# Kernel optimization log

Hardware: AMD Instinct MI355X
Metric: run time of the kernel (lower is better)

## Reference

```python
import jax, jax.numpy as jnp
import numpy as np

EPS = 1e-5  # torch nn.LayerNorm default

def layer_norm(x, g, b):
    mu = jnp.mean(x, axis=-1, keepdims=True)
    var = jnp.mean((x - mu) ** 2, axis=-1, keepdims=True)  # biased, as torch
    return (x - mu) * jax.lax.rsqrt(var + EPS) * g + b

def quantum_circuit(v):
    # RX(v_w) per wire -> <Z_w> = cos(v_w); RZ(params) is diagonal phase (no effect
    # on Z probabilities); CNOT chain makes bit w = XOR of bits 0..w, hence
    # <Z_w> = prod_{k<=w} cos(v_k). Exact closed form of the PennyLane circuit.
    return jnp.cumprod(jnp.cos(v), axis=-1)

def setup_inputs() -> dict:
    key = jax.random.key(0)
    ks = jax.random.split(key, 8)
    B, T, C, H = 4, 2048, 1024, 16
    dk = C // H           # n_qubits_transformer
    nq_ffn, ffn_dim = 16, 4096
    return {
        "x": jax.random.normal(ks[0], (B, T, C), dtype=jnp.float32) * 0.5,
        "attn_circuit_params": jax.random.normal(ks[1], (H, dk), dtype=jnp.float32),
        "ffn_circuit_params": jax.random.normal(ks[2], (nq_ffn,), dtype=jnp.float32),
        "w1": jax.random.normal(ks[3], (ffn_dim, nq_ffn), dtype=jnp.float32) * 0.1,
        "b1": jnp.zeros((ffn_dim,), dtype=jnp.float32),
        "w2": jax.random.normal(ks[4], (C, ffn_dim), dtype=jnp.float32) * 0.02,
        "b2": jnp.zeros((C,), dtype=jnp.float32),
        "gamma1": jnp.ones((C,), dtype=jnp.float32),
        "beta1": jnp.zeros((C,), dtype=jnp.float32),
        "gamma2": jnp.ones((C,), dtype=jnp.float32),
        "beta2": jnp.zeros((C,), dtype=jnp.float32),
    }

def reference(x, attn_circuit_params, ffn_circuit_params, w1, b1, w2, b2,
              gamma1, beta1, gamma2, beta2):
    B, T, C = x.shape
    H, dk = attn_circuit_params.shape  # dk == n_qubits_transformer == C // H
    nq = ffn_circuit_params.shape[0]
    # --- quantum attention: per-head circuit over d_k wires (RZ params drop out) ---
    xh = x.reshape(B, T, H, dk)
    attn_out = quantum_circuit(xh).reshape(B, T, C)
    x1 = layer_norm(x + attn_out, gamma1, beta1)  # dropout = identity (eval)
    # --- quantum FFN: circuit on first nq channels of each token ---
    q = quantum_circuit(x1[..., :nq])                      # [B,T,nq]
    h = jnp.einsum('btq,fq->btf', q, w1) + b1              # [B,T,ffn_dim]
    ffn_out = jnp.einsum('btf,cf->btc', jax.nn.relu(h), w2) + b2
    return layer_norm(x1 + ffn_out, gamma2, beta2)
```

## Files before the change

### kernel.cpp

```cpp
#include <hip/hip_runtime.h>

#define M_TOK 8192
#define C_DIM 1024
#define F_DIM 4096
#define NQ    16

typedef __attribute__((ext_vector_type(8))) short short8v;
typedef __attribute__((ext_vector_type(4))) float f32x4;

typedef __attribute__((address_space(1))) void as1_void;
typedef __attribute__((address_space(3))) void as3_void;

__device__ __forceinline__ void gld_lds16(const void* g, void* l) {
  __builtin_amdgcn_global_load_lds((as1_void*)g, (as3_void*)l, 16, 0, 0);
}

__device__ __forceinline__ unsigned short f2bf(float f) {
  unsigned int u = __float_as_uint(f);
  u += 0x7FFFu + ((u >> 16) & 1u);
  return (unsigned short)(u >> 16);
}

__device__ __forceinline__ void mfma_16x16x32_bf16(f32x4& d, short8v a, short8v b) {
  asm("v_mfma_f32_16x16x32_bf16 %0, %1, %2, %0" : "+v"(d) : "v"(a), "v"(b));
}

__global__ __launch_bounds__(256) void k_attn_ln1(
    const float* __restrict__ x, const float* __restrict__ g1,
    const float* __restrict__ be1, float* __restrict__ x1,
    float* __restrict__ qf) {
  const int row  = blockIdx.x;
  const int tid  = threadIdx.x;
  const int lane = tid & 63;
  const int w    = tid >> 6;
  const float* xr = x + (size_t)row * C_DIM;

  float y[4];
  float s1 = 0.f, s2 = 0.f;
#pragma unroll
  for (int hi = 0; hi < 4; ++hi) {
    const int idx = (w * 4 + hi) * 64 + lane;
    const float v = xr[idx];
    float p = cosf(v);
#pragma unroll
    for (int off = 1; off < 64; off <<= 1) {
      const float up = __shfl_up(p, off, 64);
      if (lane >= off) p *= up;
    }
    const float yy = v + p;
    y[hi] = yy;
    s1 += yy;
    s2 += yy * yy;
  }
#pragma unroll
  for (int off = 32; off; off >>= 1) {
    s1 += __shfl_xor(s1, off, 64);
    s2 += __shfl_xor(s2, off, 64);
  }
  __shared__ float red[8];
  if (lane == 0) { red[w] = s1; red[4 + w] = s2; }
  __syncthreads();
  s1 = red[0] + red[1] + red[2] + red[3];
  s2 = red[4] + red[5] + red[6] + red[7];
  const float mu  = s1 * (1.f / C_DIM);
  const float var = s2 * (1.f / C_DIM) - mu * mu;
  const float rs  = rsqrtf(var + 1e-5f);

  float* x1r = x1 + (size_t)row * C_DIM;
#pragma unroll
  for (int hi = 0; hi < 4; ++hi) {
    const int idx = (w * 4 + hi) * 64 + lane;
    const float xv = (y[hi] - mu) * rs * g1[idx] + be1[idx];
    x1r[idx] = xv;
    if (w == 0 && hi == 0) {
      const float c = cosf(xv);
      float run = 1.f, mine = 0.f;
#pragma unroll
      for (int k = 0; k < NQ; ++k) {
        const float ck = __shfl(c, k, 64);
        run *= ck;
        if (lane == k) mine = run;
      }
      if (lane < NQ) qf[(size_t)row * NQ + lane] = mine;
    }
  }
}

__global__ __launch_bounds__(256) void k_w2cast(const float* __restrict__ w2,
                                                unsigned short* __restrict__ w2b) {
  const int n4 = C_DIM * F_DIM / 4;
  for (int i = blockIdx.x * 256 + threadIdx.x; i < n4; i += gridDim.x * 256) {
    const float4 v = ((const float4*)w2)[i];
    unsigned long long pk = (unsigned long long)f2bf(v.x)
                          | ((unsigned long long)f2bf(v.y) << 16)
                          | ((unsigned long long)f2bf(v.z) << 32)
                          | ((unsigned long long)f2bf(v.w) << 48);
    ((unsigned long long*)w2b)[i] = pk;
  }
}

__global__ __launch_bounds__(256) void k_ffn1(
    const float* __restrict__ qf, const float* __restrict__ w1,
    const float* __restrict__ b1, unsigned short* __restrict__ R) {
  const int tid  = threadIdx.x;
  const int lane = tid & 63;
  const int wv   = tid >> 6;
  const int r16  = lane & 15;
  const int hk   = lane >> 4;
  const int mb   = blockIdx.x * 16;
  const int fb   = blockIdx.y * 64 + wv * 16;

  short8v a = short8v{0,0,0,0,0,0,0,0};
  short8v b = short8v{0,0,0,0,0,0,0,0};
  if (hk < 2) {
    const float* qa = qf + (size_t)(mb + r16) * NQ + hk * 8;
    const float4 a0 = *(const float4*)(qa);
    const float4 a1 = *(const float4*)(qa + 4);
    a[0] = (short)f2bf(a0.x); a[1] = (short)f2bf(a0.y);
    a[2] = (short)f2bf(a0.z); a[3] = (short)f2bf(a0.w);
    a[4] = (short)f2bf(a1.x); a[5] = (short)f2bf(a1.y);
    a[6] = (short)f2bf(a1.z); a[7] = (short)f2bf(a1.w);
    const float* wb = w1 + (size_t)(fb + r16) * NQ + hk * 8;
    const float4 b0 = *(const float4*)(wb);
    const float4 b1v = *(const float4*)(wb + 4);
    b[0] = (short)f2bf(b0.x); b[1] = (short)f2bf(b0.y);
    b[2] = (short)f2bf(b0.z); b[3] = (short)f2bf(b0.w);
    b[4] = (short)f2bf(b1v.x); b[5] = (short)f2bf(b1v.y);
    b[6] = (short)f2bf(b1v.z); b[7] = (short)f2bf(b1v.w);
  }

  f32x4 acc = {0.f, 0.f, 0.f, 0.f};
  mfma_16x16x32_bf16(acc, a, b);

  const int f = fb + r16;
  const float bn = b1[f];
#pragma unroll
  for (int r = 0; r < 4; ++r) {
    const int m = mb + hk * 4 + r;
    R[(size_t)m * F_DIM + f] = f2bf(fmaxf(acc[r] + bn, 0.f));
  }
}

#define BM 128
#define BN 128
#define BK 32
#define NT (F_DIM / BK)

__global__ __launch_bounds__(256) void k_gemm(
    const unsigned short* __restrict__ R, const unsigned short* __restrict__ W2,
    const float* __restrict__ b2, float* __restrict__ xio, int m_off) {
  __shared__ unsigned short As[2][BM * BK];
  __shared__ unsigned short Bs[2][BN * BK];
  const int tid = threadIdx.x;
  const int m0 = blockIdx.x * BM;
  const int n0 = blockIdx.y * BN;
  const unsigned short* Ag = R + (size_t)m0 * F_DIM;
  const unsigned short* Bg = W2 + (size_t)n0 * F_DIM;
  const int lrow = tid >> 2;
  const int lcol = (tid & 3) * 8;

  const int lane = tid & 63;
  const int wv = tid >> 6;
  const int wr = wv >> 1, wc = wv & 1;
  const int r16 = lane & 15;
  const int hk = lane >> 4;

  f32x4 acc[4][4];
  const f32x4 fzero = {0.f, 0.f, 0.f, 0.f};
#pragma unroll
  for (int i = 0; i < 4; ++i)
#pragma unroll
    for (int j = 0; j < 4; ++j) acc[i][j] = fzero;

  auto stage = [&](int buf, int t) {
    const int k0 = t * BK;
#pragma unroll
    for (int h = 0; h < 2; ++h) {
      gld_lds16(Ag + (size_t)(h * 64 + lrow) * F_DIM + k0 + lcol,
                &As[buf][h * 2048 + tid * 8]);
      gld_lds16(Bg + (size_t)(h * 64 + lrow) * F_DIM + k0 + lcol,
                &Bs[buf][h * 2048 + tid * 8]);
    }
  };

  stage(0, 0);
  asm volatile("s_waitcnt vmcnt(0)" ::: "memory");
  __builtin_amdgcn_s_barrier();
  __builtin_amdgcn_sched_barrier(0);

  for (int t = 0; t < NT; ++t) {
    const int cur = t & 1;
    if (t + 1 < NT) stage(cur ^ 1, t + 1);
    short8v a[4], b[4];
#pragma unroll
    for (int i = 0; i < 4; ++i)
      a[i] = *(const short8v*)&As[cur][(wr * 64 + i * 16 + r16) * BK + hk * 8];
#pragma unroll
    for (int j = 0; j < 4; ++j)
      b[j] = *(const short8v*)&Bs[cur][(wc * 64 + j * 16 + r16) * BK + hk * 8];
#pragma unroll
    for (int i = 0; i < 4; ++i)
#pragma unroll
      for (int j = 0; j < 4; ++j)
        mfma_16x16x32_bf16(acc[i][j], a[i], b[j]);
    asm volatile("s_waitcnt vmcnt(0)" ::: "memory");
    __builtin_amdgcn_s_barrier();
    __builtin_amdgcn_sched_barrier(0);
  }

#pragma unroll
  for (int i = 0; i < 4; ++i) {
    const int gm = m_off + m0 + wr * 64 + i * 16 + hk * 4;
#pragma unroll
    for (int j = 0; j < 4; ++j) {
      const int n = n0 + wc * 64 + j * 16 + r16;
      const float bn = b2[n];
#pragma unroll
      for (int r = 0; r < 4; ++r) {
        const size_t off = (size_t)(gm + r) * C_DIM + n;
        xio[off] = acc[i][j][r] + bn + xio[off];
      }
    }
  }
}

__global__ __launch_bounds__(256) void k_ln2(float* __restrict__ y,
                                             const float* __restrict__ g2,
                                             const float* __restrict__ be2) {
  const int row = blockIdx.x;
  const int tid = threadIdx.x;
  float* yr = y + (size_t)row * C_DIM;
  const float4 v = ((const float4*)yr)[tid];
  float s1 = v.x + v.y + v.z + v.w;
  float s2 = v.x * v.x + v.y * v.y + v.z * v.z + v.w * v.w;
#pragma unroll
  for (int off = 32; off; off >>= 1) {
    s1 += __shfl_xor(s1, off, 64);
    s2 += __shfl_xor(s2, off, 64);
  }
  __shared__ float red[8];
  const int lane = tid & 63, w = tid >> 6;
  if (lane == 0) { red[w] = s1; red[4 + w] = s2; }
  __syncthreads();
  s1 = red[0] + red[1] + red[2] + red[3];
  s2 = red[4] + red[5] + red[6] + red[7];
  const float mu  = s1 * (1.f / C_DIM);
  const float var = s2 * (1.f / C_DIM) - mu * mu;
  const float rs  = rsqrtf(var + 1e-5f);
  const float4 g = ((const float4*)g2)[tid];
  const float4 b = ((const float4*)be2)[tid];
  float4 o;
  o.x = (v.x - mu) * rs * g.x + b.x;
  o.y = (v.y - mu) * rs * g.y + b.y;
  o.z = (v.z - mu) * rs * g.z + b.z;
  o.w = (v.w - mu) * rs * g.w + b.w;
  ((float4*)yr)[tid] = o;
}

extern "C" void kernel_launch(void* const* d_in, const int* in_sizes, int n_in,
                              void* d_out, int out_size, void* d_ws, size_t ws_size,
                              hipStream_t stream) {
  const float* x   = (const float*)d_in[0];
  const float* w1  = (const float*)d_in[3];
  const float* b1  = (const float*)d_in[4];
  const float* w2  = (const float*)d_in[5];
  const float* b2  = (const float*)d_in[6];
  const float* g1  = (const float*)d_in[7];
  const float* be1 = (const float*)d_in[8];
  const float* g2  = (const float*)d_in[9];
  const float* be2 = (const float*)d_in[10];
  float* out = (float*)d_out;

  char* ws = (char*)d_ws;
  float* qf = (float*)ws;
  unsigned short* w2b = (unsigned short*)(ws + 512 * 1024);
  const size_t rbase = 512 * 1024 + (size_t)8 * 1024 * 1024;
  unsigned short* Rb = (unsigned short*)(ws + rbase);

  int cm = M_TOK;
  const size_t avail = (ws_size > rbase) ? ws_size - rbase : 0;
  const size_t need = (size_t)M_TOK * F_DIM * 2;
  if (avail < need) {
    size_t rows = (avail / ((size_t)F_DIM * 2)) & ~(size_t)127;
    cm = (rows < 128) ? 128 : (int)rows;
  }

  k_attn_ln1<<<M_TOK, 256, 0, stream>>>(x, g1, be1, out, qf);
  k_w2cast<<<2048, 256, 0, stream>>>(w2, w2b);
  for (int c0 = 0; c0 < M_TOK; c0 += cm) {
    const int cur = (M_TOK - c0 < cm) ? (M_TOK - c0) : cm;
    k_ffn1<<<dim3(cur / 16, F_DIM / 64), 256, 0, stream>>>(
        qf + (size_t)c0 * NQ, w1, b1, Rb);
    k_gemm<<<dim3(cur / BM, C_DIM / BN), 256, 0, stream>>>(Rb, w2b, b2, out, c0);
  }
  k_ln2<<<M_TOK, 256, 0, stream>>>(out, g2, be2);
}
```

Baseline: 159.5 us.

## Rework FFN2 GEMM: 256x128x64 tiles, 8 waves, triple-buffered swizzled LDS pipeline

```diff
diff --git a/kernel.cpp b/kernel.cpp
--- a/kernel.cpp
+++ b/kernel.cpp
@@ -141,29 +141,32 @@
   }
 }
 
-#define BM 128
+#define BM 256
 #define BN 128
-#define BK 32
+#define BK 64
 #define NT (F_DIM / BK)
-
-__global__ __launch_bounds__(256) void k_gemm(
+#define ATILE (BM * BK)
+#define BTILE (BN * BK)
+#define TILE3 (ATILE + BTILE)
+
+__global__ __launch_bounds__(512) void k_gemm(
     const unsigned short* __restrict__ R, const unsigned short* __restrict__ W2,
     const float* __restrict__ b2, float* __restrict__ xio, int m_off) {
-  __shared__ unsigned short As[2][BM * BK];
-  __shared__ unsigned short Bs[2][BN * BK];
+  __shared__ unsigned short L[3 * TILE3];
   const int tid = threadIdx.x;
   const int m0 = blockIdx.x * BM;
   const int n0 = blockIdx.y * BN;
   const unsigned short* Ag = R + (size_t)m0 * F_DIM;
   const unsigned short* Bg = W2 + (size_t)n0 * F_DIM;
-  const int lrow = tid >> 2;
-  const int lcol = (tid & 3) * 8;
 
   const int lane = tid & 63;
-  const int wv = tid >> 6;
-  const int wr = wv >> 1, wc = wv & 1;
+  const int wv  = tid >> 6;
+  const int wr  = wv >> 1;
+  const int wc  = wv & 1;
   const int r16 = lane & 15;
-  const int hk = lane >> 4;
+  const int hk  = lane >> 4;
+  const int ar0 = wr * 64 + r16;
+  const int br0 = wc * 64 + r16;
 
   f32x4 acc[4][4];
   const f32x4 fzero = {0.f, 0.f, 0.f, 0.f};
@@ -172,40 +175,102 @@
 #pragma unroll
     for (int j = 0; j < 4; ++j) acc[i][j] = fzero;
 
-  auto stage = [&](int buf, int t) {
-    const int k0 = t * BK;
-#pragma unroll
-    for (int h = 0; h < 2; ++h) {
-      gld_lds16(Ag + (size_t)(h * 64 + lrow) * F_DIM + k0 + lcol,
-                &As[buf][h * 2048 + tid * 8]);
-      gld_lds16(Bg + (size_t)(h * 64 + lrow) * F_DIM + k0 + lcol,
-                &Bs[buf][h * 2048 + tid * 8]);
-    }
+  auto stageA = [&](int c, int t, int l) {
+    const int idx = l * 512 + tid;
+    const int row = idx >> 3, slot = idx & 7;
+    gld_lds16(Ag + (size_t)row * F_DIM + t * BK + ((slot ^ (row & 7)) << 3),
+              &L[c * TILE3 + idx * 8]);
   };
-
-  stage(0, 0);
-  asm volatile("s_waitcnt vmcnt(0)" ::: "memory");
+  auto stageB = [&](int c, int t, int l) {
+    const int idx = l * 512 + tid;
+    const int row = idx >> 3, slot = idx & 7;
+    gld_lds16(Bg + (size_t)row * F_DIM + t * BK + ((slot ^ (row & 7)) << 3),
+              &L[c * TILE3 + ATILE + idx * 8]);
+  };
+  auto rdA = [&](int c, int row, int ks) {
+    return *(const short8v*)&L[c * TILE3 + row * BK + ((ks ^ (row & 7)) << 3)];
+  };
+  auto rdB = [&](int c, int row, int ks) {
+    return *(const short8v*)&L[c * TILE3 + ATILE + row * BK + ((ks ^ (row & 7)) << 3)];
+  };
+
+#pragma unroll
+  for (int l = 0; l < 4; ++l) stageA(0, 0, l);
+#pragma unroll
+  for (int l = 0; l < 2; ++l) stageB(0, 0, l);
+#pragma unroll
+  for (int l = 0; l < 4; ++l) stageA(1, 1, l);
+#pragma unroll
+  for (int l = 0; l < 2; ++l) stageB(1, 1, l);
+  asm volatile("s_waitcnt vmcnt(6)" ::: "memory");
   __builtin_amdgcn_s_barrier();
-  __builtin_amdgcn_sched_barrier(0);
 
   for (int t = 0; t < NT; ++t) {
-    const int cur = t & 1;
-    if (t + 1 < NT) stage(cur ^ 1, t + 1);
-    short8v a[4], b[4];
-#pragma unroll
-    for (int i = 0; i < 4; ++i)
-      a[i] = *(const short8v*)&As[cur][(wr * 64 + i * 16 + r16) * BK + hk * 8];
-#pragma unroll
-    for (int j = 0; j < 4; ++j)
-      b[j] = *(const short8v*)&Bs[cur][(wc * 64 + j * 16 + r16) * BK + hk * 8];
-#pragma unroll
-    for (int i = 0; i < 4; ++i)
-#pragma unroll
-      for (int j = 0; j < 4; ++j)
-        mfma_16x16x32_bf16(acc[i][j], a[i], b[j]);
-    asm volatile("s_waitcnt vmcnt(0)" ::: "memory");
-    __builtin_amdgcn_s_barrier();
+    const int cur = t % 3;
+    const int nx2 = (t + 2) % 3;
+    const bool pf = (t + 2) < NT;
+    short8v a0, a1, b[4];
+
+    a0 = rdA(cur, ar0,      hk);
+    a1 = rdA(cur, ar0 + 16, hk);
+#pragma unroll
+    for (int j = 0; j < 4; ++j) b[j] = rdB(cur, br0 + j * 16, hk);
+    if (pf) { stageA(nx2, t + 2, 0); stageA(nx2, t + 2, 1); }
+    __builtin_amdgcn_s_barrier();
+    asm volatile("s_waitcnt lgkmcnt(0)" ::: "memory");
     __builtin_amdgcn_sched_barrier(0);
+    __builtin_amdgcn_s_setprio(1);
+#pragma unroll
+    for (int j = 0; j < 4; ++j) mfma_16x16x32_bf16(acc[0][j], a0, b[j]);
+#pragma unroll
+    for (int j = 0; j < 4; ++j) mfma_16x16x32_bf16(acc[1][j], a1, b[j]);
+    __builtin_amdgcn_s_setprio(0);
+    __builtin_amdgcn_s_barrier();
+
+    a0 = rdA(cur, ar0 + 32, hk);
+    a1 = rdA(cur, ar0 + 48, hk);
+    if (pf) { stageA(nx2, t + 2, 2); stageA(nx2, t + 2, 3); }
+    __builtin_amdgcn_s_barrier();
+    asm volatile("s_waitcnt lgkmcnt(0)" ::: "memory");
+    __builtin_amdgcn_sched_barrier(0);
+    __builtin_amdgcn_s_setprio(1);
+#pragma unroll
+    for (int j = 0; j < 4; ++j) mfma_16x16x32_bf16(acc[2][j], a0, b[j]);
+#pragma unroll
+    for (int j = 0; j < 4; ++j) mfma_16x16x32_bf16(acc[3][j], a1, b[j]);
+    __builtin_amdgcn_s_setprio(0);
+    __builtin_amdgcn_s_barrier();
+
+    a0 = rdA(cur, ar0,      hk + 4);
+    a1 = rdA(cur, ar0 + 16, hk + 4);
+#pragma unroll
+    for (int j = 0; j < 4; ++j) b[j] = rdB(cur, br0 + j * 16, hk + 4);
+    if (pf) { stageB(nx2, t + 2, 0); stageB(nx2, t + 2, 1); }
+    __builtin_amdgcn_s_barrier();
+    asm volatile("s_waitcnt lgkmcnt(0)" ::: "memory");
+    __builtin_amdgcn_sched_barrier(0);
+    __builtin_amdgcn_s_setprio(1);
+#pragma unroll
+    for (int j = 0; j < 4; ++j) mfma_16x16x32_bf16(acc[0][j], a0, b[j]);
+#pragma unroll
+    for (int j = 0; j < 4; ++j) mfma_16x16x32_bf16(acc[1][j], a1, b[j]);
+    __builtin_amdgcn_s_setprio(0);
+    __builtin_amdgcn_s_barrier();
+
+    a0 = rdA(cur, ar0 + 32, hk + 4);
+    a1 = rdA(cur, ar0 + 48, hk + 4);
+    __builtin_amdgcn_s_barrier();
+    asm volatile("s_waitcnt lgkmcnt(0)" ::: "memory");
+    __builtin_amdgcn_sched_barrier(0);
+    __builtin_amdgcn_s_setprio(1);
+#pragma unroll
+    for (int j = 0; j < 4; ++j) mfma_16x16x32_bf16(acc[2][j], a0, b[j]);
+#pragma unroll
+    for (int j = 0; j < 4; ++j) mfma_16x16x32_bf16(acc[3][j], a1, b[j]);
+    __builtin_amdgcn_s_setprio(0);
+    if (pf) asm volatile("s_waitcnt vmcnt(6)" ::: "memory");
+    else    asm volatile("s_waitcnt vmcnt(0)" ::: "memory");
+    __builtin_amdgcn_s_barrier();
   }
 
 #pragma unroll
@@ -281,8 +346,8 @@
   const size_t avail = (ws_size > rbase) ? ws_size - rbase : 0;
   const size_t need = (size_t)M_TOK * F_DIM * 2;
   if (avail < need) {
-    size_t rows = (avail / ((size_t)F_DIM * 2)) & ~(size_t)127;
-    cm = (rows < 128) ? 128 : (int)rows;
+    size_t rows = (avail / ((size_t)F_DIM * 2)) & ~(size_t)255;
+    cm = (rows < 256) ? 256 : (int)rows;
   }
 
   k_attn_ln1<<<M_TOK, 256, 0, stream>>>(x, g1, be1, out, qf);
@@ -291,7 +356,7 @@
     const int cur = (M_TOK - c0 < cm) ? (M_TOK - c0) : cm;
     k_ffn1<<<dim3(cur / 16, F_DIM / 64), 256, 0, stream>>>(
         qf + (size_t)c0 * NQ, w1, b1, Rb);
-    k_gemm<<<dim3(cur / BM, C_DIM / BN), 256, 0, stream>>>(Rb, w2b, b2, out, c0);
+    k_gemm<<<dim3(cur / BM, C_DIM / BN), 512, 0, stream>>>(Rb, w2b, b2, out, c0);
   }
   k_ln2<<<M_TOK, 256, 0, stream>>>(out, g2, be2);
 }
```

Measured after the change: 146.6 us. 8.0% less time.
